# Kernel tuning notes

Hardware: AMD Instinct MI355X
Metric: run time of the kernel (lower is better)

The kernel has to match this reference:

```python
import jax, jax.numpy as jnp
import numpy as np

TOP_P = 0.9  # forward default arg, fixed to exercise the top-p path


def setup_inputs() -> dict:
    key = jax.random.key(0)
    k1, k2 = jax.random.split(key)
    B, V = 128, 128000
    logits = jax.random.normal(k1, (B, V), dtype=jnp.float32) * 2.0
    # temperatures in [0.5, 1.5) to avoid divide-by-near-zero
    temperatures = jax.random.uniform(k2, (B,), dtype=jnp.float32, minval=0.5, maxval=1.5)
    return {"logits": logits, "temperatures": temperatures, "top_k": 50}


def reference(logits, temperatures, top_k):
    B, V = logits.shape
    neg_inf = jnp.float32(-jnp.inf)

    # temperature scale + softmax
    scaled = logits.astype(jnp.float32) / temperatures[:, None]
    probs = jax.nn.softmax(scaled, axis=-1)  # (B, V)

    brow = jnp.arange(B)[:, None]

    # top-k filter: keep top-k probs, fill rest with -inf (matches torch scatter into full(-inf))
    if top_k > 0:
        k = min(top_k, V)
        vals, idx = jax.lax.top_k(probs, k)  # (B, k)
        probs = jnp.full_like(probs, neg_inf).at[brow, idx].set(vals)

    # top-p (nucleus) filter: sort desc, cumsum, mask tail beyond top_p (always keep first)
    if TOP_P < 1.0:
        order = jnp.argsort(-probs, axis=-1)              # descending order indices (-inf sorts last)
        sorted_probs = jnp.take_along_axis(probs, order, axis=-1)
        cum = jnp.cumsum(sorted_probs, axis=-1)
        remove = cum > TOP_P
        remove = remove.at[:, 0].set(False)
        sorted_probs = jnp.where(remove, neg_inf, sorted_probs)
        probs = probs.at[brow, order].set(sorted_probs)   # scatter back to original positions

    # Gumbel-max-style sampling: argmax(probs / Exp(1) noise), noise clamped to >= 1e-10
    kn = jax.random.fold_in(jax.random.key(0), 1)
    noise = jnp.maximum(jax.random.exponential(kn, probs.shape, dtype=jnp.float32), 1e-10)
    return jnp.argmax(probs / noise, axis=-1)  # (B,) int tokens
```

## Files before the change

kernel.cpp:

```cpp
#include <hip/hip_runtime.h>
#include <stdint.h>
#include <limits.h>

#define THREEFRY_PARTITIONABLE 1

#define NTK   512
#define NWAVE (NTK/64)
#define NBUCK 4096
#define BPT   (NBUCK/NTK)
#define CAPS  256
#define CAPG  2048
#define CAPF  512
#define KMAX  512
#define SMAX  32
#define CHUNK_TARGET 16384

#define NT1   1024
#define CAP1  4096

#if __has_builtin(__builtin_amdgcn_exp2f)
#define FAST_EXP2(x) __builtin_amdgcn_exp2f(x)
#else
#define FAST_EXP2(x) exp2f(x)
#endif

__device__ __forceinline__ uint32_t rotl32(uint32_t v, int r) {
  return (v << r) | (v >> (32 - r));
}
__device__ __forceinline__ void tfround(uint32_t& x0, uint32_t& x1, int r) {
  x0 += x1; x1 = rotl32(x1, r); x1 ^= x0;
}
__device__ __forceinline__ void threefry2x32(uint32_t k0, uint32_t k1,
                                             uint32_t x0, uint32_t x1,
                                             uint32_t& o0, uint32_t& o1) {
  uint32_t k2 = k0 ^ k1 ^ 0x1BD11BDAu;
  x0 += k0; x1 += k1;
  tfround(x0,x1,13); tfround(x0,x1,15); tfround(x0,x1,26); tfround(x0,x1,6);
  x0 += k1; x1 += k2 + 1u;
  tfround(x0,x1,17); tfround(x0,x1,29); tfround(x0,x1,16); tfround(x0,x1,24);
  x0 += k2; x1 += k0 + 2u;
  tfround(x0,x1,13); tfround(x0,x1,15); tfround(x0,x1,26); tfround(x0,x1,6);
  x0 += k0; x1 += k1 + 3u;
  tfround(x0,x1,17); tfround(x0,x1,29); tfround(x0,x1,16); tfround(x0,x1,24);
  x0 += k1; x1 += k2 + 4u;
  tfround(x0,x1,13); tfround(x0,x1,15); tfround(x0,x1,26); tfround(x0,x1,6);
  x0 += k2; x1 += k0 + 5u;
  o0 = x0; o1 = x1;
}
__device__ __forceinline__ float jax_noise(uint32_t kn0, uint32_t kn1,
                                           unsigned long long i,
                                           unsigned long long total) {
  uint32_t o0, o1, bits;
#if THREEFRY_PARTITIONABLE
  threefry2x32(kn0, kn1, (uint32_t)(i >> 32), (uint32_t)(i & 0xFFFFFFFFull), o0, o1);
  bits = o0 ^ o1;
#else
  unsigned long long H = total >> 1;
  if (i < H) { threefry2x32(kn0, kn1, (uint32_t)i, (uint32_t)(i + H), o0, o1); bits = o0; }
  else       { threefry2x32(kn0, kn1, (uint32_t)(i - H), (uint32_t)i, o0, o1); bits = o1; }
#endif
  float u = __uint_as_float((bits >> 9) | 0x3f800000u) - 1.0f;
  float e = -log1pf(-u);
  return fmaxf(e, 1e-10f);
}
__device__ __forceinline__ uint32_t fkey(float f) {
  uint32_t u = __float_as_uint(f);
  return u ^ ((u >> 31) ? 0xFFFFFFFFu : 0x80000000u);
}
__device__ __forceinline__ float unfkey_floor(uint32_t keyT) {
  if (keyT == 0u) return -INFINITY;
  return __uint_as_float((keyT & 0x80000000u) ? (keyT ^ 0x80000000u) : ~keyT);
}
__device__ __forceinline__ int clamp_k(int k) {
  if (k < 1) k = 1;
  if (k > KMAX) k = KMAX;
  return k;
}

__device__ __forceinline__ void block_kth_bucket(uint32_t* hist, uint32_t* wtot,
                                                 int* beta_sh, int k,
                                                 int tid, int lane, int wave) {
  const int base = tid * BPT;
  uint32_t tsum = 0;
#pragma unroll
  for (int j = 0; j < BPT; j++) tsum += hist[base + j];
  uint32_t incl = tsum;
  for (int off = 1; off < 64; off <<= 1) {
    uint32_t v = __shfl_down(incl, off);
    if (lane + off < 64) incl += v;
  }
  if (lane == 0) wtot[wave] = incl;
  __syncthreads();
  uint32_t above = incl - tsum;
  for (int w = wave + 1; w < NWAVE; w++) above += wtot[w];
  if (above < (uint32_t)k && above + tsum >= (uint32_t)k) {
    uint32_t run = above;
    for (int j = BPT - 1; j >= 0; j--) {
      run += hist[base + j];
      if (run >= (uint32_t)k) { *beta_sh = base + j; break; }
    }
  }
  __syncthreads();
}

__global__ __launch_bounds__(NTK)
void sampler_stream(const float* __restrict__ logits,
                    const float* __restrict__ temps,
                    const int* __restrict__ topk_ptr,
                    float* __restrict__ msArr,
                    double* __restrict__ dsumArr,
                    int* __restrict__ cntArr,
                    float2* __restrict__ pairs,
                    int B, int V, int S, int chunk) {
  const int blk = blockIdx.x;
  const int b = blk / S, sp = blk % S;
  const int tid = threadIdx.x, lane = tid & 63, wave = tid >> 6;

  __shared__ uint32_t hist[NBUCK];
  __shared__ float wm[NWAVE];
  __shared__ double wsum[NWAVE];
  __shared__ uint32_t wtot[NWAVE];
  __shared__ int beta_sh, cnum_sh;

  if (tid == 0) { beta_sh = 0; cnum_sh = 0; }
  for (int i = tid; i < NBUCK; i += NTK) hist[i] = 0;

  const float T = temps[b];
  const float cf = (float)(1.4426950408889634 / (double)T);
  const int k = clamp_k(*topk_ptr);

  const int start = sp * chunk;
  const int end = min(start + chunk, V);
  const float* row = logits + (size_t)b * (size_t)V;
  const int n = (end > start) ? (end - start) : 0;
  const int n4 = n >> 2;
  const float4* row4 = (const float4*)(row + start);

  float v0 = -INFINITY, v1 = -INFINITY;
  int   i0 = 0, i1 = 0;
  float acc0 = 0.f, acc1 = 0.f;

  auto proc = [&](float f, int idx) {
    bool gt0 = f > v0;
    bool gt1 = f > v1;
    float nv1 = gt0 ? v0 : (gt1 ? f : v1);
    int   ni1 = gt0 ? i0 : (gt1 ? idx : i1);
    v1 = nv1; i1 = ni1;
    v0 = gt0 ? f : v0;
    i0 = gt0 ? idx : i0;
  };
  auto proc4 = [&](float4 f, int vb) {
    proc(f.x, vb); proc(f.y, vb + 1); proc(f.z, vb + 2); proc(f.w, vb + 3);
    acc0 += FAST_EXP2(f.x * cf) + FAST_EXP2(f.z * cf);
    acc1 += FAST_EXP2(f.y * cf) + FAST_EXP2(f.w * cf);
  };

  int i = tid;
  for (; i + 3 * NTK < n4; i += 4 * NTK) {
    float4 fa = row4[i];
    float4 fb = row4[i + NTK];
    float4 fc = row4[i + 2 * NTK];
    float4 fd = row4[i + 3 * NTK];
    proc4(fa, start + i * 4);
    proc4(fb, start + (i + NTK) * 4);
    proc4(fc, start + (i + 2 * NTK) * 4);
    proc4(fd, start + (i + 3 * NTK) * 4);
  }
  for (; i < n4; i += NTK) {
    float4 fa = row4[i];
    proc4(fa, start + i * 4);
  }
  for (int v = start + n4 * 4 + tid; v < end; v += NTK) {
    float f = row[v];
    proc(f, v);
    acc0 += FAST_EXP2(f * cf);
  }

  float bm = v0;
  for (int off = 32; off; off >>= 1)
    bm = fmaxf(bm, __shfl_down(bm, off));
  if (lane == 0) wm[wave] = bm;

  double ds = (double)acc0 + (double)acc1;
  for (int off = 32; off; off >>= 1)
    ds += __shfl_down(ds, off);
  if (lane == 0) wsum[wave] = ds;

  if (v0 != -INFINITY) atomicAdd(&hist[fkey(v0) >> 20], 1u);
  __syncthreads();

  if (tid == 0) {
    float m_sp = wm[0];
#pragma unroll
    for (int w = 1; w < NWAVE; w++) m_sp = fmaxf(m_sp, wm[w]);
    msArr[blk] = m_sp;
    double t = 0.0;
    for (int w = 0; w < NWAVE; w++) t += wsum[w];
    dsumArr[blk] = t;
  }

  block_kth_bucket(hist, wtot, &beta_sh, k, tid, lane, wave);

  const float fT = unfkey_floor((uint32_t)beta_sh << 20);
  float2* myp = pairs + (size_t)blk * CAPS;

  if (v0 >= fT) {
    if (v1 >= fT) {
      for (int i2 = tid; i2 < n4; i2 += NTK) {
        float4 f = row4[i2];
        const int vb = start + i2 * 4;
        if (f.x >= fT) { int p = atomicAdd(&cnum_sh, 1); if (p < CAPS) myp[p] = make_float2(f.x, __int_as_float(vb)); }
        if (f.y >= fT) { int p = atomicAdd(&cnum_sh, 1); if (p < CAPS) myp[p] = make_float2(f.y, __int_as_float(vb + 1)); }
        if (f.z >= fT) { int p = atomicAdd(&cnum_sh, 1); if (p < CAPS) myp[p] = make_float2(f.z, __int_as_float(vb + 2)); }
        if (f.w >= fT) { int p = atomicAdd(&cnum_sh, 1); if (p < CAPS) myp[p] = make_float2(f.w, __int_as_float(vb + 3)); }
      }
      for (int v = start + n4 * 4 + tid; v < end; v += NTK) {
        float f = row[v];
        if (f >= fT) { int p = atomicAdd(&cnum_sh, 1); if (p < CAPS) myp[p] = make_float2(f, __int_as_float(v)); }
      }
    } else {
      int p = atomicAdd(&cnum_sh, 1);
      if (p < CAPS) myp[p] = make_float2(v0, __int_as_float(i0));
    }
  }
  __syncthreads();
  if (tid == 0) cntArr[blk] = min(cnum_sh, CAPS);
}

__global__ __launch_bounds__(NTK)
void sampler_finalize(const float* __restrict__ temps,
                      const int* __restrict__ topk_ptr,
                      const float* __restrict__ msArr,
                      const double* __restrict__ dsumArr,
                      const int* __restrict__ cntArr,
                      const float2* __restrict__ pairs,
                      int* __restrict__ out,
                      int B, int V, int S) {
  const int b = blockIdx.x;
  const int tid = threadIdx.x, lane = tid & 63, wave = tid >> 6;

  __shared__ uint32_t hist[NBUCK];
  __shared__ float gv[CAPG];
  __shared__ int   gi[CAPG];
  __shared__ float c2v[CAPF];
  __shared__ int   c2i[CAPF];
  __shared__ float c2p[CAPF];
  __shared__ float sv[KMAX];
  __shared__ int   si[KMAX];
  __shared__ float sc[KMAX];
  __shared__ int   offL[SMAX + 1];
  __shared__ int   cnL[SMAX];
  __shared__ float msL[SMAX];
  __shared__ double dsL[SMAX];
  __shared__ uint32_t wtot[NWAVE];
  __shared__ int beta_sh, cnt2_sh, L_sh;
  __shared__ float m_sh, D_sh;

  const int k = clamp_k(*topk_ptr);
  const float T = temps[b];

  if (tid == 0) { beta_sh = 0; cnt2_sh = 0; }
  if (tid < S) {
    msL[tid] = msArr[b * S + tid];
    dsL[tid] = dsumArr[b * S + tid];
    int c = cntArr[b * S + tid];
    cnL[tid] = (c < CAPS) ? c : CAPS;
  }
  for (int i = tid; i < NBUCK; i += NTK) hist[i] = 0;
  __syncthreads();

  if (tid == 0) {
    int acc = 0;
    for (int j = 0; j < S; j++) { offL[j] = acc; acc += cnL[j]; }
    offL[S] = acc;
  }

  if (wave == 1 || (NWAVE == 1 && wave == 0)) {
    float msp = (lane < S) ? msL[lane] : -INFINITY;
    float mg = msp;
    for (int off = 32; off; off >>= 1)
      mg = fmaxf(mg, __shfl_down(mg, off));
    mg = __shfl(mg, 0);
    double term = (lane < S) ? dsL[lane] : 0.0;
    for (int off = 32; off; off >>= 1)
      term += __shfl_down(term, off);
    if (lane == 0) {
      const double cd = 1.4426950408889634 / (double)T;
      D_sh = (float)(term * exp2(-(double)mg * cd));
      m_sh = mg / T;
    }
  }
  __syncthreads();

  const int TC = min(offL[S], CAPG);

  for (int t = tid; t < TC; t += NTK) {
    int j = 0;
#pragma unroll
    for (int jj = 1; jj <= SMAX; jj++)
      if (jj <= S) j += (t >= offL[jj]);
    float2 pr = pairs[(size_t)(b * S + j) * CAPS + (t - offL[j])];
    gv[t] = pr.x;
    gi[t] = __float_as_int(pr.y);
    atomicAdd(&hist[fkey(pr.x) >> 20], 1u);
  }
  __syncthreads();

  block_kth_bucket(hist, wtot, &beta_sh, k, tid, lane, wave);

  const float fT = unfkey_floor((uint32_t)beta_sh << 20);
  for (int t = tid; t < TC; t += NTK) {
    float val = gv[t];
    if (val >= fT) {
      int pos = atomicAdd(&cnt2_sh, 1);
      if (pos < CAPF) { c2v[pos] = val; c2i[pos] = gi[t]; }
    }
  }
  __syncthreads();

  const int C = min(cnt2_sh, CAPF);
  const float m = m_sh, D = D_sh;
  for (int i = tid; i < C; i += NTK)
    c2p[i] = expf(c2v[i] / T - m) / D;
  __syncthreads();

  for (int i = tid; i < C; i += NTK) {
    float pi = c2p[i];
    int   ii = c2i[i];
    int r = 0;
    for (int j = 0; j < C; j++) {
      float pj = c2p[j];
      r += (pj > pi) || (pj == pi && c2i[j] < ii);
    }
    if (r < k) { sv[r] = pi; si[r] = ii; }
  }
  __syncthreads();

  const int kk = (k < C) ? k : C;
  if (tid == 0) {
    float cum = 0.f;
    int L = 1;
    for (int j = 0; j < kk; j++) {
      cum += sv[j];
      if (j == 0) continue;
      if (cum <= 0.9f) L = j + 1; else break;
    }
    L_sh = L;
  }
  __syncthreads();

  const int L = L_sh;
  {
    uint32_t kn0, kn1;
    threefry2x32(0u, 0u, 0u, 1u, kn0, kn1);
    unsigned long long total = (unsigned long long)B * (unsigned long long)V;
    for (int j = tid; j < L; j += NTK) {
      unsigned long long flat = (unsigned long long)b * (unsigned long long)V
                              + (unsigned long long)si[j];
      sc[j] = sv[j] / jax_noise(kn0, kn1, flat, total);
    }
  }
  __syncthreads();

  if (tid == 0) {
    float bs = -1.0f;
    int   bi = INT_MAX;
    for (int j = 0; j < L; j++) {
      if (sc[j] > bs || (sc[j] == bs && si[j] < bi)) { bs = sc[j]; bi = si[j]; }
    }
    out[b] = bi;
  }
}

__global__ __launch_bounds__(NT1, 1)
void sampler_fallback(const float* __restrict__ logits,
                      const float* __restrict__ temps,
                      const int* __restrict__ topk_ptr,
                      int* __restrict__ out,
                      int B, int V) {
  const int b    = blockIdx.x;
  const int tid  = threadIdx.x;
  const int lane = tid & 63;
  const int wave = tid >> 6;

  __shared__ uint32_t hist[NBUCK];
  __shared__ float    cand_p[CAP1];
  __shared__ int      cand_i[CAP1];
  __shared__ float    wmax[16];
  __shared__ double   wsum[16];
  __shared__ float    svals[KMAX];
  __shared__ int      sidx[KMAX];
  __shared__ float    m_sh, D_sh;
  __shared__ int      beta_sh, cnum_sh, L_sh;

  const float T = temps[b];
  const float* row = logits + (size_t)b * (size_t)V;
  int k = clamp_k(*topk_ptr);
  if (k > V) k = V;

  if (tid == 0) { beta_sh = 1; cnum_sh = 0; }
  for (int i = tid; i < NBUCK; i += NT1) hist[i] = 0;
  __syncthreads();

  float t8[8];
#pragma unroll
  for (int j = 0; j < 8; j++) t8[j] = -INFINITY;
  float mymax = -INFINITY;
  for (int v = tid; v < V; v += NT1) {
    float s = row[v] / T;
    mymax = fmaxf(mymax, s);
    if (s > t8[0]) {
      t8[0] = s;
#pragma unroll
      for (int j = 1; j < 8; j++)
        if (t8[j-1] > t8[j]) { float tmp = t8[j]; t8[j] = t8[j-1]; t8[j-1] = tmp; }
    }
  }
  for (int off = 32; off > 0; off >>= 1)
    mymax = fmaxf(mymax, __shfl_down(mymax, off));
  if (lane == 0) wmax[wave] = mymax;
#pragma unroll
  for (int j = 0; j < 8; j++)
    if (t8[j] != -INFINITY) atomicAdd(&hist[fkey(t8[j]) >> 20], 1u);
  __syncthreads();
  if (tid == 0) {
    float m = -INFINITY;
    for (int w = 0; w < 16; w++) m = fmaxf(m, wmax[w]);
    m_sh = m;
  }
  if (wave == 1) {
    int base = lane * 64;
    uint32_t ssum = 0;
    for (int j = 0; j < 64; j++) ssum += hist[base + ((j + lane) & 63)];
    uint32_t incl = ssum;
    for (int off = 1; off < 64; off <<= 1) {
      uint32_t vv = __shfl_down(incl, off);
      if (lane + off < 64) incl += vv;
    }
    uint32_t higher = incl - ssum;
    if (higher < (uint32_t)k && incl >= (uint32_t)k) {
      uint32_t run = higher;
      for (int j = 63; j >= 0; j--) {
        run += hist[base + j];
        if (run >= (uint32_t)k) { beta_sh = base + j; break; }
      }
    }
  }
  __syncthreads();
  const float m = m_sh;
  const uint32_t keyT = (uint32_t)((beta_sh >= 1 ? beta_sh - 1 : 0)) << 20;
  double dsum = 0.0;
  for (int v = tid; v < V; v += NT1) {
    float s = row[v] / T;
    float e = expf(s - m);
    dsum += (double)e;
    if (fkey(s) >= keyT) {
      int pos = atomicAdd(&cnum_sh, 1);
      if (pos < CAP1) { cand_p[pos] = e; cand_i[pos] = v; }
    }
  }
  for (int off = 32; off > 0; off >>= 1)
    dsum += __shfl_down(dsum, off);
  if (lane == 0) wsum[wave] = dsum;
  __syncthreads();
  if (tid == 0) {
    double t = 0.0;
    for (int w = 0; w < 16; w++) t += wsum[w];
    D_sh = (float)t;
  }
  __syncthreads();
  const float D = D_sh;
  const int C = (cnum_sh < CAP1) ? cnum_sh : CAP1;
  for (int i = tid; i < C; i += NT1) cand_p[i] = cand_p[i] / D;
  __syncthreads();
  for (int i = tid; i < C; i += NT1) {
    float pi = cand_p[i];
    int   ii = cand_i[i];
    int r = 0;
    for (int j = 0; j < C; j++) {
      float pj = cand_p[j];
      r += (pj > pi) || (pj == pi && cand_i[j] < ii);
    }
    if (r < k) { svals[r] = pi; sidx[r] = ii; }
  }
  __syncthreads();
  if (tid == 0) {
    float cum = 0.f;
    int L = 1;
    for (int j = 0; j < k; j++) {
      cum += svals[j];
      if (j == 0) continue;
      if (cum <= 0.9f) L = j + 1; else break;
    }
    L_sh = L;
  }
  __syncthreads();
  const int L = L_sh;
  if (tid < L) {
    uint32_t kn0, kn1;
    threefry2x32(0u, 0u, 0u, 1u, kn0, kn1);
    unsigned long long total = (unsigned long long)B * (unsigned long long)V;
    unsigned long long flat = (unsigned long long)b * (unsigned long long)V
                            + (unsigned long long)sidx[tid];
    cand_p[tid] = svals[tid] / jax_noise(kn0, kn1, flat, total);
  }
  __syncthreads();
  if (tid == 0) {
    float bs = -1.0f;
    int   bi = INT_MAX;
    for (int j = 0; j < L; j++) {
      if (cand_p[j] > bs || (cand_p[j] == bs && sidx[j] < bi)) { bs = cand_p[j]; bi = sidx[j]; }
    }
    out[b] = bi;
  }
}

extern "C" void kernel_launch(void* const* d_in, const int* in_sizes, int n_in,
                              void* d_out, int out_size, void* d_ws, size_t ws_size,
                              hipStream_t stream) {
  const float* logits = (const float*)d_in[0];
  const float* temps  = (const float*)d_in[1];
  const int*   topk   = (const int*)d_in[2];
  int* out = (int*)d_out;

  int B = in_sizes[1];
  int V = in_sizes[0] / B;

  int S = (V + CHUNK_TARGET - 1) / CHUNK_TARGET;
  if (S > SMAX) S = SMAX;
  if (S < 1) S = 1;
  size_t need;
  for (;;) {
    need = (size_t)B * S * (sizeof(double) + sizeof(float) + sizeof(int))
         + (size_t)B * S * CAPS * sizeof(float2);
    if (need <= ws_size || S <= 2) break;
    S >>= 1;
  }

  if (ws_size < need || S < 2) {
    sampler_fallback<<<dim3(B), dim3(NT1), 0, stream>>>(logits, temps, topk, out, B, V);
    return;
  }

  int chunk = (((V + S - 1) / S) + 3) & ~3;

  double* dsumArr = (double*)d_ws;
  float*  msArr   = (float*)(dsumArr + (size_t)B * S);
  int*    cntArr  = (int*)(msArr + (size_t)B * S);
  float2* pairs   = (float2*)(cntArr + (size_t)B * S);

  sampler_stream<<<dim3(B * S), dim3(NTK), 0, stream>>>(
      logits, temps, topk, msArr, dsumArr, cntArr, pairs, B, V, S, chunk);
  sampler_finalize<<<dim3(B), dim3(NTK), 0, stream>>>(
      temps, topk, msArr, dsumArr, cntArr, pairs, out, B, V, S);
}
```

Baseline: 118.9 us.

## Fuse finalize into stream kernel via last-block-per-row atomic counter

Merges the separate finalize kernel into the streaming kernel: each chunk block bumps a per-row atomic counter, and the last block for a row runs the top-k/top-p selection and sampling. This removes a kernel launch and the gap between the two kernels, but adds a memset launch and raises shared memory per block, which may cut occupancy for the streaming phase. It also simplifies the per-element running second-max update to a fmax/fmin form, and re-reads candidate pairs from global memory instead of staging them in shared arrays, which drops the old cap on gathered candidates.

```diff
diff --git a/kernel.cpp b/kernel.cpp
--- a/kernel.cpp
+++ b/kernel.cpp
@@ -9,7 +9,6 @@
 #define NBUCK 4096
 #define BPT   (NBUCK/NTK)
 #define CAPS  256
-#define CAPG  2048
 #define CAPF  512
 #define KMAX  512
 #define SMAX  32
@@ -104,14 +103,16 @@
 }
 
 __global__ __launch_bounds__(NTK)
-void sampler_stream(const float* __restrict__ logits,
-                    const float* __restrict__ temps,
-                    const int* __restrict__ topk_ptr,
-                    float* __restrict__ msArr,
-                    double* __restrict__ dsumArr,
-                    int* __restrict__ cntArr,
-                    float2* __restrict__ pairs,
-                    int B, int V, int S, int chunk) {
+void sampler_fused(const float* __restrict__ logits,
+                   const float* __restrict__ temps,
+                   const int* __restrict__ topk_ptr,
+                   int* __restrict__ rowCnt,
+                   float* __restrict__ msArr,
+                   double* __restrict__ dsumArr,
+                   int* __restrict__ cntArr,
+                   float2* __restrict__ pairs,
+                   int* __restrict__ out,
+                   int B, int V, int S, int chunk) {
   const int blk = blockIdx.x;
   const int b = blk / S, sp = blk % S;
   const int tid = threadIdx.x, lane = tid & 63, wave = tid >> 6;
@@ -120,7 +121,19 @@
   __shared__ float wm[NWAVE];
   __shared__ double wsum[NWAVE];
   __shared__ uint32_t wtot[NWAVE];
-  __shared__ int beta_sh, cnum_sh;
+  __shared__ int beta_sh, cnum_sh, last_sh;
+  __shared__ float c2v[CAPF];
+  __shared__ int   c2i[CAPF];
+  __shared__ float c2p[CAPF];
+  __shared__ float sv[KMAX];
+  __shared__ int   si[KMAX];
+  __shared__ float sc[KMAX];
+  __shared__ int   offL[SMAX + 1];
+  __shared__ int   cnL[SMAX];
+  __shared__ float msL[SMAX];
+  __shared__ double dsL[SMAX];
+  __shared__ int cnt2_sh, L_sh;
+  __shared__ float m_sh, D_sh;
 
   if (tid == 0) { beta_sh = 0; cnum_sh = 0; }
   for (int i = tid; i < NBUCK; i += NTK) hist[i] = 0;
@@ -137,17 +150,14 @@
   const float4* row4 = (const float4*)(row + start);
 
   float v0 = -INFINITY, v1 = -INFINITY;
-  int   i0 = 0, i1 = 0;
+  int   i0 = 0;
   float acc0 = 0.f, acc1 = 0.f;
 
   auto proc = [&](float f, int idx) {
-    bool gt0 = f > v0;
-    bool gt1 = f > v1;
-    float nv1 = gt0 ? v0 : (gt1 ? f : v1);
-    int   ni1 = gt0 ? i0 : (gt1 ? idx : i1);
-    v1 = nv1; i1 = ni1;
-    v0 = gt0 ? f : v0;
-    i0 = gt0 ? idx : i0;
+    v1 = fmaxf(v1, fminf(f, v0));
+    bool gt = f > v0;
+    v0 = gt ? f : v0;
+    i0 = gt ? idx : i0;
   };
   auto proc4 = [&](float4 f, int vb) {
     proc(f.x, vb); proc(f.y, vb + 1); proc(f.z, vb + 2); proc(f.w, vb + 3);
@@ -224,40 +234,16 @@
     }
   }
   __syncthreads();
-  if (tid == 0) cntArr[blk] = min(cnum_sh, CAPS);
-}
-
-__global__ __launch_bounds__(NTK)
-void sampler_finalize(const float* __restrict__ temps,
-                      const int* __restrict__ topk_ptr,
-                      const float* __restrict__ msArr,
-                      const double* __restrict__ dsumArr,
-                      const int* __restrict__ cntArr,
-                      const float2* __restrict__ pairs,
-                      int* __restrict__ out,
-                      int B, int V, int S) {
-  const int b = blockIdx.x;
-  const int tid = threadIdx.x, lane = tid & 63, wave = tid >> 6;
-
-  __shared__ uint32_t hist[NBUCK];
-  __shared__ float gv[CAPG];
-  __shared__ int   gi[CAPG];
-  __shared__ float c2v[CAPF];
-  __shared__ int   c2i[CAPF];
-  __shared__ float c2p[CAPF];
-  __shared__ float sv[KMAX];
-  __shared__ int   si[KMAX];
-  __shared__ float sc[KMAX];
-  __shared__ int   offL[SMAX + 1];
-  __shared__ int   cnL[SMAX];
-  __shared__ float msL[SMAX];
-  __shared__ double dsL[SMAX];
-  __shared__ uint32_t wtot[NWAVE];
-  __shared__ int beta_sh, cnt2_sh, L_sh;
-  __shared__ float m_sh, D_sh;
-
-  const int k = clamp_k(*topk_ptr);
-  const float T = temps[b];
+
+  if (tid == 0) {
+    cntArr[blk] = min(cnum_sh, CAPS);
+    __threadfence();
+    int old = atomicAdd(&rowCnt[b], 1);
+    __threadfence();
+    last_sh = (old == S - 1);
+  }
+  __syncthreads();
+  if (!last_sh) return;
 
   if (tid == 0) { beta_sh = 0; cnt2_sh = 0; }
   if (tid < S) {
@@ -266,7 +252,7 @@
     int c = cntArr[b * S + tid];
     cnL[tid] = (c < CAPS) ? c : CAPS;
   }
-  for (int i = tid; i < NBUCK; i += NTK) hist[i] = 0;
+  for (int i2 = tid; i2 < NBUCK; i2 += NTK) hist[i2] = 0;
   __syncthreads();
 
   if (tid == 0) {
@@ -275,7 +261,7 @@
     offL[S] = acc;
   }
 
-  if (wave == 1 || (NWAVE == 1 && wave == 0)) {
+  if (wave == 1) {
     float msp = (lane < S) ? msL[lane] : -INFINITY;
     float mg = msp;
     for (int off = 32; off; off >>= 1)
@@ -292,7 +278,7 @@
   }
   __syncthreads();
 
-  const int TC = min(offL[S], CAPG);
+  const int TC = offL[S];
 
   for (int t = tid; t < TC; t += NTK) {
     int j = 0;
@@ -300,33 +286,35 @@
     for (int jj = 1; jj <= SMAX; jj++)
       if (jj <= S) j += (t >= offL[jj]);
     float2 pr = pairs[(size_t)(b * S + j) * CAPS + (t - offL[j])];
-    gv[t] = pr.x;
-    gi[t] = __float_as_int(pr.y);
     atomicAdd(&hist[fkey(pr.x) >> 20], 1u);
   }
   __syncthreads();
 
   block_kth_bucket(hist, wtot, &beta_sh, k, tid, lane, wave);
 
-  const float fT = unfkey_floor((uint32_t)beta_sh << 20);
+  const float fT2 = unfkey_floor((uint32_t)beta_sh << 20);
   for (int t = tid; t < TC; t += NTK) {
-    float val = gv[t];
-    if (val >= fT) {
+    int j = 0;
+#pragma unroll
+    for (int jj = 1; jj <= SMAX; jj++)
+      if (jj <= S) j += (t >= offL[jj]);
+    float2 pr = pairs[(size_t)(b * S + j) * CAPS + (t - offL[j])];
+    if (pr.x >= fT2) {
       int pos = atomicAdd(&cnt2_sh, 1);
-      if (pos < CAPF) { c2v[pos] = val; c2i[pos] = gi[t]; }
+      if (pos < CAPF) { c2v[pos] = pr.x; c2i[pos] = __float_as_int(pr.y); }
     }
   }
   __syncthreads();
 
   const int C = min(cnt2_sh, CAPF);
   const float m = m_sh, D = D_sh;
-  for (int i = tid; i < C; i += NTK)
-    c2p[i] = expf(c2v[i] / T - m) / D;
-  __syncthreads();
-
-  for (int i = tid; i < C; i += NTK) {
-    float pi = c2p[i];
-    int   ii = c2i[i];
+  for (int i2 = tid; i2 < C; i2 += NTK)
+    c2p[i2] = expf(c2v[i2] / T - m) / D;
+  __syncthreads();
+
+  for (int i2 = tid; i2 < C; i2 += NTK) {
+    float pi = c2p[i2];
+    int   ii = c2i[i2];
     int r = 0;
     for (int j = 0; j < C; j++) {
       float pj = c2p[j];
@@ -529,9 +517,11 @@
   int S = (V + CHUNK_TARGET - 1) / CHUNK_TARGET;
   if (S > SMAX) S = SMAX;
   if (S < 1) S = 1;
+  size_t rcBytes = ((size_t)B * sizeof(int) + 7) & ~(size_t)7;
   size_t need;
   for (;;) {
-    need = (size_t)B * S * (sizeof(double) + sizeof(float) + sizeof(int))
+    need = rcBytes
+         + (size_t)B * S * (sizeof(double) + sizeof(float) + sizeof(int))
          + (size_t)B * S * CAPS * sizeof(float2);
     if (need <= ws_size || S <= 2) break;
     S >>= 1;
@@ -544,13 +534,15 @@
 
   int chunk = (((V + S - 1) / S) + 3) & ~3;
 
-  double* dsumArr = (double*)d_ws;
+  int*    rowCnt  = (int*)d_ws;
+  double* dsumArr = (double*)((char*)d_ws + rcBytes);
   float*  msArr   = (float*)(dsumArr + (size_t)B * S);
   int*    cntArr  = (int*)(msArr + (size_t)B * S);
   float2* pairs   = (float2*)(cntArr + (size_t)B * S);
 
-  sampler_stream<<<dim3(B * S), dim3(NTK), 0, stream>>>(
-      logits, temps, topk, msArr, dsumArr, cntArr, pairs, B, V, S, chunk);
-  sampler_finalize<<<dim3(B), dim3(NTK), 0, stream>>>(
-      temps, topk, msArr, dsumArr, cntArr, pairs, out, B, V, S);
-}
+  hipMemsetAsync(rowCnt, 0, (size_t)B * sizeof(int), stream);
+
+  sampler_fused<<<dim3(B * S), dim3(NTK), 0, stream>>>(
+      logits, temps, topk, rowCnt, msArr, dsumArr, cntArr, pairs, out,
+      B, V, S, chunk);
+}
```

Result: slower. 172.9 us (+45.4%).

## Keep chunk in registers for reuse in candidate pass; simplify top-2 tracking

Applied to the files above, without the earlier changes.

The block's slice of the row (up to 8 float4 per thread) is loaded into registers up front. The stats pass and the threshold-candidate gather both read from these registers, so the second global read of the chunk is avoided. The second-largest tracker drops its index and becomes a branch-free fmax/fmin update. In exchange, register pressure per thread rises, which may lower occupancy.

```diff
diff --git a/kernel.cpp b/kernel.cpp
--- a/kernel.cpp
+++ b/kernel.cpp
@@ -6,6 +6,7 @@
 
 #define NTK   512
 #define NWAVE (NTK/64)
+#define RD    8
 #define NBUCK 4096
 #define BPT   (NBUCK/NTK)
 #define CAPS  256
@@ -136,18 +137,22 @@
   const int n4 = n >> 2;
   const float4* row4 = (const float4*)(row + start);
 
+  float4 r[RD];
+#pragma unroll
+  for (int it = 0; it < RD; it++) {
+    const int i = tid + it * NTK;
+    if (i < n4) r[it] = row4[i];
+  }
+
   float v0 = -INFINITY, v1 = -INFINITY;
-  int   i0 = 0, i1 = 0;
+  int   i0 = 0;
   float acc0 = 0.f, acc1 = 0.f;
 
   auto proc = [&](float f, int idx) {
-    bool gt0 = f > v0;
-    bool gt1 = f > v1;
-    float nv1 = gt0 ? v0 : (gt1 ? f : v1);
-    int   ni1 = gt0 ? i0 : (gt1 ? idx : i1);
-    v1 = nv1; i1 = ni1;
-    v0 = gt0 ? f : v0;
-    i0 = gt0 ? idx : i0;
+    v1 = fmaxf(v1, fminf(f, v0));
+    bool gt = f > v0;
+    v0 = gt ? f : v0;
+    i0 = gt ? idx : i0;
   };
   auto proc4 = [&](float4 f, int vb) {
     proc(f.x, vb); proc(f.y, vb + 1); proc(f.z, vb + 2); proc(f.w, vb + 3);
@@ -155,20 +160,14 @@
     acc1 += FAST_EXP2(f.y * cf) + FAST_EXP2(f.w * cf);
   };
 
-  int i = tid;
-  for (; i + 3 * NTK < n4; i += 4 * NTK) {
-    float4 fa = row4[i];
-    float4 fb = row4[i + NTK];
-    float4 fc = row4[i + 2 * NTK];
-    float4 fd = row4[i + 3 * NTK];
-    proc4(fa, start + i * 4);
-    proc4(fb, start + (i + NTK) * 4);
-    proc4(fc, start + (i + 2 * NTK) * 4);
-    proc4(fd, start + (i + 3 * NTK) * 4);
-  }
-  for (; i < n4; i += NTK) {
-    float4 fa = row4[i];
-    proc4(fa, start + i * 4);
+#pragma unroll
+  for (int it = 0; it < RD; it++) {
+    const int i = tid + it * NTK;
+    if (i < n4) proc4(r[it], start + i * 4);
+  }
+  for (int i = tid + RD * NTK; i < n4; i += NTK) {
+    float4 f = row4[i];
+    proc4(f, start + i * 4);
   }
   for (int v = start + n4 * 4 + tid; v < end; v += NTK) {
     float f = row[v];
@@ -206,9 +205,21 @@
 
   if (v0 >= fT) {
     if (v1 >= fT) {
-      for (int i2 = tid; i2 < n4; i2 += NTK) {
-        float4 f = row4[i2];
-        const int vb = start + i2 * 4;
+#pragma unroll
+      for (int it = 0; it < RD; it++) {
+        const int i = tid + it * NTK;
+        if (i < n4) {
+          float4 f = r[it];
+          const int vb = start + i * 4;
+          if (f.x >= fT) { int p = atomicAdd(&cnum_sh, 1); if (p < CAPS) myp[p] = make_float2(f.x, __int_as_float(vb)); }
+          if (f.y >= fT) { int p = atomicAdd(&cnum_sh, 1); if (p < CAPS) myp[p] = make_float2(f.y, __int_as_float(vb + 1)); }
+          if (f.z >= fT) { int p = atomicAdd(&cnum_sh, 1); if (p < CAPS) myp[p] = make_float2(f.z, __int_as_float(vb + 2)); }
+          if (f.w >= fT) { int p = atomicAdd(&cnum_sh, 1); if (p < CAPS) myp[p] = make_float2(f.w, __int_as_float(vb + 3)); }
+        }
+      }
+      for (int i = tid + RD * NTK; i < n4; i += NTK) {
+        float4 f = row4[i];
+        const int vb = start + i * 4;
         if (f.x >= fT) { int p = atomicAdd(&cnum_sh, 1); if (p < CAPS) myp[p] = make_float2(f.x, __int_as_float(vb)); }
         if (f.y >= fT) { int p = atomicAdd(&cnum_sh, 1); if (p < CAPS) myp[p] = make_float2(f.y, __int_as_float(vb + 1)); }
         if (f.z >= fT) { int p = atomicAdd(&cnum_sh, 1); if (p < CAPS) myp[p] = make_float2(f.z, __int_as_float(vb + 2)); }
```

New measurement: 119.3 us. Within noise of the previous version (+0.3%).
